# Performance work log

Hardware: AMD Instinct MI355X
Metric: run time of the kernel (lower is better)

Reference implementation:

```python
import jax, jax.numpy as jnp
import numpy as np

B, T, D, H = 32, 512, 1024, 1024


def setup_inputs() -> dict:
    key = jax.random.key(0)
    k1, k2, k3 = jax.random.split(key, 3)
    x = jax.random.normal(k1, (B, T, D), dtype=jnp.float32)
    c0 = jnp.zeros((B, H), dtype=jnp.float32)
    h0 = jnp.zeros((B, H), dtype=jnp.float32)
    # scale weights so gates do not saturate
    Wx = jax.random.normal(k2, (D, 4 * H), dtype=jnp.float32) * 0.05
    Wh = jax.random.normal(k3, (H, 4 * H), dtype=jnp.float32) * 0.05
    b = jnp.zeros((4 * H,), dtype=jnp.float32)
    return {"x": x, "c0": c0, "h0": h0, "Wx": Wx, "Wh": Wh, "b": b}


def reference(x, c0, h0, Wx, Wh, b):
    # Flax LSTMCell: gates = x @ Wx + h @ Wh + b, split into i,f,g,o.
    # Precompute the input projection for all timesteps (one big GEMM).
    xW = jnp.einsum('btd,dg->btg', x, Wx) + b  # [B,T,4H]

    def step(carry, xw_t):
        c, h = carry
        gates = xw_t + h @ Wh  # [B,4H]
        i, f, g, o = jnp.split(gates, 4, axis=-1)
        i = jax.nn.sigmoid(i)
        f = jax.nn.sigmoid(f)
        g = jnp.tanh(g)
        o = jax.nn.sigmoid(o)
        c_new = f * c + i * g
        h_new = o * jnp.tanh(c_new)
        return (c_new, h_new), h_new

    (cT, hT), ys = jax.lax.scan(step, (c0, h0), jnp.swapaxes(xW, 0, 1))
    outputs = jnp.swapaxes(ys, 0, 1)  # [B,T,H]
    return outputs, (cT, hT)
```

## Files before the change

kernel.cpp:

```cpp
#include <hip/hip_runtime.h>
#include <cstddef>

#define NB 32
#define NT 512
#define ND 1024
#define NH 1024
#define NG 4096
#define GRID 256

typedef unsigned short ushortT;
typedef unsigned long long u64;
typedef __attribute__((ext_vector_type(8))) short short8;
typedef __attribute__((ext_vector_type(4))) float f32x4;
typedef __attribute__((ext_vector_type(4))) unsigned uint4v;

#define GLL16(g, l) __builtin_amdgcn_global_load_lds(                      \
    (const __attribute__((address_space(1))) void*)(g),                    \
    (__attribute__((address_space(3))) void*)(l), 16, 0, 0)

__device__ __forceinline__ ushortT f2bf(float f) {
    union { float f; unsigned u; } v; v.f = f;
    unsigned r = v.u + 0x7FFFu + ((v.u >> 16) & 1u);
    return (ushortT)(r >> 16);
}
__device__ __forceinline__ float bf2f(ushortT u) {
    union { unsigned u; float f; } v; v.u = (unsigned)u << 16; return v.f;
}

__device__ __forceinline__ float pick4(float a0, float a1, float a2, float a3, int s) {
    float lo = (s & 1) ? a1 : a0;
    float hi = (s & 1) ? a3 : a2;
    return (s & 2) ? hi : lo;
}

__device__ __forceinline__ float fsigmoid(float x) {
    return __builtin_amdgcn_rcpf(1.f + __expf(-x));
}
__device__ __forceinline__ float ftanh(float x) {
    float xc = fminf(fmaxf(x, -15.f), 15.f);
    float e  = __expf(-2.f * xc);
    return (1.f - e) * __builtin_amdgcn_rcpf(1.f + e);
}

__global__ __launch_bounds__(256) void cast_bf16(const float* __restrict__ src,
                                                 ushortT* __restrict__ dst, int n4)
{
    int i = blockIdx.x * 256 + threadIdx.x;
    if (i < n4) {
        float4 v = ((const float4*)src)[i];
        ushort4 o;
        o.x = f2bf(v.x); o.y = f2bf(v.y); o.z = f2bf(v.z); o.w = f2bf(v.w);
        ((ushort4*)dst)[i] = o;
    }
}

__global__ __launch_bounds__(256) void transpose_cast(
    const float* __restrict__ src, ushortT* __restrict__ dst, int permute)
{
    __shared__ ushortT tile[64][66];
    const int c0 = blockIdx.x * 64, r0 = blockIdx.y * 64;
    const int cc = threadIdx.x & 63, rq = threadIdx.x >> 6;
    #pragma unroll
    for (int ps = 0; ps < 16; ++ps) {
        int r = ps * 4 + rq;
        tile[cc][r] = f2bf(src[(size_t)(r0 + r) * NG + c0 + cc]);
    }
    __syncthreads();
    #pragma unroll
    for (int ps = 0; ps < 16; ++ps) {
        int cl = ps * 4 + rq;
        int n  = c0 + cl;
        int drow = permute ? ((((n & 1023) >> 2) << 4) | ((n >> 10) << 2) | (n & 3))
                           : n;
        dst[(size_t)drow * 1024 + r0 + cc] = tile[cl][cc];
    }
}

__global__ __launch_bounds__(256) void gemm_xw_mfma(
    const ushortT* __restrict__ xb,
    const ushortT* __restrict__ wxT,
    const float* __restrict__ bias,
    ushortT* __restrict__ XWPb,
    int t0, int Tc, int tcsh)
{
    __shared__ ushortT As[128 * 32];
    __shared__ ushortT Bs[128 * 32];

    const int tid  = threadIdx.x;
    const int lane = tid & 63;
    const int wv   = tid >> 6;
    const int wr   = wv >> 1, wc = wv & 1;
    const int n0   = blockIdx.x * 128;
    const int m0   = blockIdx.y * 128;

    const int c1 = tid, c2 = tid + 256;
    const int rm1 = m0 + (c1 >> 2), rm2 = m0 + (c2 >> 2);
    const int xr1 = ((rm1 >> tcsh) * NT) + t0 + (rm1 & (Tc - 1));
    const int xr2 = ((rm2 >> tcsh) * NT) + t0 + (rm2 & (Tc - 1));
    const ushortT* ap1 = xb + (size_t)xr1 * ND + (c1 & 3) * 8;
    const ushortT* ap2 = xb + (size_t)xr2 * ND + (c2 & 3) * 8;
    const ushortT* bp1 = wxT + (size_t)(n0 + (c1 >> 2)) * ND + (c1 & 3) * 8;
    const ushortT* bp2 = wxT + (size_t)(n0 + (c2 >> 2)) * ND + (c2 & 3) * 8;

    f32x4 acc[4][4];
    #pragma unroll
    for (int m = 0; m < 4; ++m)
        #pragma unroll
        for (int n = 0; n < 4; ++n) acc[m][n] = (f32x4){0.f, 0.f, 0.f, 0.f};

    const int arow_base = (wr * 64 + (lane & 15)) * 32 + (lane >> 4) * 8;
    const int brow_base = (wc * 64 + (lane & 15)) * 32 + (lane >> 4) * 8;

    for (int k0 = 0; k0 < ND; k0 += 32) {
        __syncthreads();
        GLL16(ap1 + k0, &As[c1 * 8]);
        GLL16(ap2 + k0, &As[c2 * 8]);
        GLL16(bp1 + k0, &Bs[c1 * 8]);
        GLL16(bp2 + k0, &Bs[c2 * 8]);
        __syncthreads();
        short8 af[4], bf[4];
        #pragma unroll
        for (int m = 0; m < 4; ++m)
            af[m] = *(const short8*)&As[arow_base + m * 16 * 32];
        #pragma unroll
        for (int n = 0; n < 4; ++n)
            bf[n] = *(const short8*)&Bs[brow_base + n * 16 * 32];
        #pragma unroll
        for (int m = 0; m < 4; ++m)
            #pragma unroll
            for (int n = 0; n < 4; ++n)
                acc[m][n] = __builtin_amdgcn_mfma_f32_16x16x32_bf16(
                    af[m], bf[n], acc[m][n], 0, 0, 0);
    }

    #pragma unroll
    for (int n = 0; n < 4; ++n) {
        int col = n0 + wc * 64 + n * 16 + (lane & 15);
        int pc  = (((col & 1023) >> 2) << 4) | ((col >> 10) << 2) | (col & 3);
        float bs = bias[col];
        #pragma unroll
        for (int m = 0; m < 4; ++m) {
            #pragma unroll
            for (int r = 0; r < 4; ++r) {
                int rm = m0 + wr * 64 + m * 16 + (lane >> 4) * 4 + r;
                int b  = rm >> tcsh, tr = rm & (Tc - 1);
                XWPb[((size_t)tr * NB + b) * NG + pc] = f2bf(acc[m][n][r] + bs);
            }
        }
    }
}

__global__ __launch_bounds__(512) void lstm_persist(
    const ushortT* __restrict__ XWPb,
    const ushortT* __restrict__ whpT,
    unsigned* __restrict__ hb0,
    unsigned* __restrict__ hb1,
    const float* __restrict__ cinit,
    float* __restrict__ cT,
    float* __restrict__ out,
    float* __restrict__ hT,
    unsigned* __restrict__ flags,
    int t0, int Tc)
{
    __shared__ float red[2][16 * 272];

    const int tid  = threadIdx.x;
    const int lane = tid & 63;
    const int w    = tid >> 6;
    const int grp  = blockIdx.x & 1;
    const int s    = blockIdx.x >> 1;

    const int lo = lane & 15;
    const int hi = lane >> 4;

    const int rrow  = tid >> 5;
    const int col32 = tid & 31;
    const int rct   = col32 >> 4, rc16 = col32 & 15;
    const int gq    = (col32 >> 2) & 3;
    const int uu    = (col32 >> 4) * 4 + (col32 & 3);
    const int j     = s * 8 + uu;
    const int brow  = grp * 16 + rrow;

    short8 Bf[2][4];
    #pragma unroll
    for (int ct = 0; ct < 2; ++ct)
        #pragma unroll
        for (int ks = 0; ks < 4; ++ks)
            Bf[ct][ks] = *(const short8*)(whpT
                + (size_t)(s * 32 + ct * 16 + lo) * NH + w * 128 + ks * 32 + hi * 8);

    float creg = cinit[(size_t)brow * NH + j];

    const size_t abase64 = (size_t)lo * 256 + w * 32 + hi * 2;

    unsigned* const gf = flags + grp * 1024;
    const u64* fp = (const u64*)(gf + 128 * w + 2 * lane);
    unsigned* const fmine = gf + s * 8 + w;

    ushortT xvr = XWPb[(size_t)brow * NG + s * 32 + col32];

    const int tend = t0 + Tc;
    for (int t = t0; t < tend; ++t) {
        const int trel = t - t0;
        const int par  = t & 1;
        const unsigned* hR = ((t & 1) ? hb0 : hb1) + grp * 8192;
        unsigned*       hW = ((t & 1) ? hb1 : hb0) + grp * 8192;

        if (trel) {
            const unsigned tgt = (unsigned)trel;
            for (int it = 0; it < (1 << 17); ++it) {
                u64 v = __hip_atomic_load(fp, __ATOMIC_RELAXED,
                                          __HIP_MEMORY_SCOPE_AGENT);
                bool ok = ((unsigned)v >= tgt) && ((unsigned)(v >> 32) >= tgt);
                if (__all(ok)) break;
            }
        }

        const u64* ap = (const u64*)hR + abase64;
        u64 q0, q1;
        uint4v d0, d1, d2, d3;
        q0 = __hip_atomic_load(ap + 0,  __ATOMIC_RELAXED, __HIP_MEMORY_SCOPE_AGENT);
        q1 = __hip_atomic_load(ap + 1,  __ATOMIC_RELAXED, __HIP_MEMORY_SCOPE_AGENT);
        d0 = (uint4v){(unsigned)q0, (unsigned)(q0 >> 32), (unsigned)q1, (unsigned)(q1 >> 32)};
        q0 = __hip_atomic_load(ap + 8,  __ATOMIC_RELAXED, __HIP_MEMORY_SCOPE_AGENT);
        q1 = __hip_atomic_load(ap + 9,  __ATOMIC_RELAXED, __HIP_MEMORY_SCOPE_AGENT);
        d1 = (uint4v){(unsigned)q0, (unsigned)(q0 >> 32), (unsigned)q1, (unsigned)(q1 >> 32)};
        q0 = __hip_atomic_load(ap + 16, __ATOMIC_RELAXED, __HIP_MEMORY_SCOPE_AGENT);
        q1 = __hip_atomic_load(ap + 17, __ATOMIC_RELAXED, __HIP_MEMORY_SCOPE_AGENT);
        d2 = (uint4v){(unsigned)q0, (unsigned)(q0 >> 32), (unsigned)q1, (unsigned)(q1 >> 32)};
        q0 = __hip_atomic_load(ap + 24, __ATOMIC_RELAXED, __HIP_MEMORY_SCOPE_AGENT);
        q1 = __hip_atomic_load(ap + 25, __ATOMIC_RELAXED, __HIP_MEMORY_SCOPE_AGENT);
        d3 = (uint4v){(unsigned)q0, (unsigned)(q0 >> 32), (unsigned)q1, (unsigned)(q1 >> 32)};

        short8 A0 = *(short8*)&d0;
        short8 A1 = *(short8*)&d1;
        short8 A2 = *(short8*)&d2;
        short8 A3 = *(short8*)&d3;

        f32x4 acc0 = (f32x4){0.f, 0.f, 0.f, 0.f};
        f32x4 acc1 = (f32x4){0.f, 0.f, 0.f, 0.f};
        acc0 = __builtin_amdgcn_mfma_f32_16x16x32_bf16(A0, Bf[0][0], acc0, 0, 0, 0);
        acc1 = __builtin_amdgcn_mfma_f32_16x16x32_bf16(A0, Bf[1][0], acc1, 0, 0, 0);
        acc0 = __builtin_amdgcn_mfma_f32_16x16x32_bf16(A1, Bf[0][1], acc0, 0, 0, 0);
        acc1 = __builtin_amdgcn_mfma_f32_16x16x32_bf16(A1, Bf[1][1], acc1, 0, 0, 0);
        acc0 = __builtin_amdgcn_mfma_f32_16x16x32_bf16(A2, Bf[0][2], acc0, 0, 0, 0);
        acc1 = __builtin_amdgcn_mfma_f32_16x16x32_bf16(A2, Bf[1][2], acc1, 0, 0, 0);
        acc0 = __builtin_amdgcn_mfma_f32_16x16x32_bf16(A3, Bf[0][3], acc0, 0, 0, 0);
        acc1 = __builtin_amdgcn_mfma_f32_16x16x32_bf16(A3, Bf[1][3], acc1, 0, 0, 0);

        #pragma unroll
        for (int r = 0; r < 4; ++r) {
            red[par][(w * 2 + 0) * 272 + (hi * 4 + r) * 17 + lo] = acc0[r];
            red[par][(w * 2 + 1) * 272 + (hi * 4 + r) * 17 + lo] = acc1[r];
        }
        __syncthreads();

        float g = bf2f(xvr);
        #pragma unroll
        for (int wv = 0; wv < 8; ++wv)
            g += red[par][(wv * 2 + rct) * 272 + rrow * 17 + rc16];

        float g4  = __shfl_xor(g, 4);
        float g8  = __shfl_xor(g, 8);
        float g12 = __shfl_xor(g, 12);

        float gi = pick4(g, g4, g8, g12, gq);
        float gf = pick4(g, g4, g8, g12, gq ^ 1);
        float gg = pick4(g, g4, g8, g12, gq ^ 2);
        float go = pick4(g, g4, g8, g12, gq ^ 3);

        float iv = fsigmoid(gi);
        float fv = fsigmoid(gf);
        float gv = ftanh(gg);
        float ov = fsigmoid(go);
        float cn = fv * creg + iv * gv;
        float hn = ov * ftanh(cn);
        creg = cn;

        float ph = __shfl_xor(hn, 1);
        const bool wl = (gq == 0) && ((col32 & 1) == 0);
        if (wl) {
            unsigned pair = (unsigned)f2bf(hn) | ((unsigned)f2bf(ph) << 16);
            __hip_atomic_store(&hW[rrow * 512 + (j >> 1)], pair,
                               __ATOMIC_RELAXED, __HIP_MEMORY_SCOPE_AGENT);
        }

        if (t != tend - 1) {
            asm volatile("s_waitcnt vmcnt(0)" ::: "memory");
            if (lane == 0)
                __hip_atomic_store(fmine, (unsigned)(trel + 1),
                                   __ATOMIC_RELAXED, __HIP_MEMORY_SCOPE_AGENT);
            if (wl)
                *(float2*)&out[((size_t)brow * NT + t) * NH + j] = make_float2(hn, ph);
            xvr = XWPb[((size_t)(trel + 1) * NB + brow) * NG + s * 32 + col32];
        } else {
            if (wl)
                *(float2*)&out[((size_t)brow * NT + t) * NH + j] = make_float2(hn, ph);
            if (gq == 0) {
                if (t == NT - 1) hT[(size_t)brow * NH + j] = hn;
                cT[(size_t)brow * NH + j] = cn;
            }
        }
    }
}

extern "C" void kernel_launch(void* const* d_in, const int* in_sizes, int n_in,
                              void* d_out, int out_size, void* d_ws, size_t ws_size,
                              hipStream_t stream) {
    const float* x    = (const float*)d_in[0];
    const float* c0   = (const float*)d_in[1];
    const float* h0   = (const float*)d_in[2];
    const float* Wx   = (const float*)d_in[3];
    const float* Wh   = (const float*)d_in[4];
    const float* bias = (const float*)d_in[5];

    float* out = (float*)d_out;
    float* cT  = out + (size_t)NB * NT * NH;
    float* hT  = cT + (size_t)NB * NH;

    ushortT* xb   = (ushortT*)d_ws;
    ushortT* wxT  = xb  + (size_t)NB * NT * ND;
    ushortT* whpT = wxT + (size_t)NG * ND;
    unsigned* hb0 = (unsigned*)(whpT + (size_t)NG * NH);
    unsigned* hb1 = hb0 + NB * NH / 2;
    unsigned* flags = hb1 + NB * NH / 2;
    ushortT* xwpb = (ushortT*)(flags + 2 * 1024);

    const size_t fixed = ((size_t)NB * NT * ND + (size_t)NG * ND + (size_t)NG * NH
                          + 2 * NB * NH) * sizeof(ushortT) + 2 * 1024 * 4 + 256;
    int Tc = 512;
    while (Tc > 4 && fixed + (size_t)NB * Tc * NG * sizeof(ushortT) > ws_size)
        Tc >>= 1;
    int tcsh = 31 - __builtin_clz(Tc);

    cast_bf16<<<(NB * NT * ND / 4 + 255) / 256, 256, 0, stream>>>(x, xb, NB * NT * ND / 4);
    cast_bf16<<<(NB * NH / 4 + 255) / 256, 256, 0, stream>>>(h0, (ushortT*)hb1, NB * NH / 4);
    transpose_cast<<<dim3(64, 16), 256, 0, stream>>>(Wx, wxT, 0);
    transpose_cast<<<dim3(64, 16), 256, 0, stream>>>(Wh, whpT, 1);

    for (int t0 = 0; t0 < NT; t0 += Tc) {
        dim3 g(NG / 128, (NB * Tc) / 128);
        gemm_xw_mfma<<<g, 256, 0, stream>>>(xb, wxT, bias, xwpb, t0, Tc, tcsh);
        hipMemsetAsync(flags, 0, 2 * 1024 * sizeof(unsigned), stream);
        lstm_persist<<<GRID, 512, 0, stream>>>(
            xwpb, whpT, hb0, hb1,
            (t0 == 0) ? c0 : (const float*)cT,
            cT, out, hT, flags, t0, Tc);
    }
}
```

Baseline: 2.312 ms.

## Repartition persistent LSTM blocks to own gate columns across both batch halves

Each persistent block now owns 16 gate columns (4 hidden units) for all 32 batch rows, instead of 32 gate columns for one 16-row batch half. Each timestep runs as two phases, one per batch half, each with its own flag wait, h-buffer half and LDS reduction. This halves the per-block recurrent weight fragments and the MFMA work per phase. The aim is to interleave the two independent batch chains so one half's wait overlaps the other's compute. In exchange it adds a second barrier and flag poll per step, serializes both chains through every block, and leaves only half the threads active in the elementwise stage.

```diff
diff --git a/kernel.cpp b/kernel.cpp
--- a/kernel.cpp
+++ b/kernel.cpp
@@ -162,144 +162,153 @@
     unsigned* __restrict__ flags,
     int t0, int Tc)
 {
-    __shared__ float red[2][16 * 272];
+    __shared__ float red[2][8 * 16 * 17];
 
     const int tid  = threadIdx.x;
     const int lane = tid & 63;
     const int w    = tid >> 6;
-    const int grp  = blockIdx.x & 1;
-    const int s    = blockIdx.x >> 1;
+    const int blk  = blockIdx.x;
 
     const int lo = lane & 15;
     const int hi = lane >> 4;
 
-    const int rrow  = tid >> 5;
-    const int col32 = tid & 31;
-    const int rct   = col32 >> 4, rc16 = col32 & 15;
-    const int gq    = (col32 >> 2) & 3;
-    const int uu    = (col32 >> 4) * 4 + (col32 & 3);
-    const int j     = s * 8 + uu;
-    const int brow  = grp * 16 + rrow;
-
-    short8 Bf[2][4];
-    #pragma unroll
-    for (int ct = 0; ct < 2; ++ct)
-        #pragma unroll
-        for (int ks = 0; ks < 4; ++ks)
-            Bf[ct][ks] = *(const short8*)(whpT
-                + (size_t)(s * 32 + ct * 16 + lo) * NH + w * 128 + ks * 32 + hi * 8);
-
-    float creg = cinit[(size_t)brow * NH + j];
-
-    const size_t abase64 = (size_t)lo * 256 + w * 32 + hi * 2;
-
-    unsigned* const gf = flags + grp * 1024;
-    const u64* fp = (const u64*)(gf + 128 * w + 2 * lane);
-    unsigned* const fmine = gf + s * 8 + w;
-
-    ushortT xvr = XWPb[(size_t)brow * NG + s * 32 + col32];
+    short8 Bf[4];
+    #pragma unroll
+    for (int ks = 0; ks < 4; ++ks)
+        Bf[ks] = *(const short8*)(whpT
+            + (size_t)(blk * 16 + lo) * NH + w * 128 + ks * 32 + hi * 8);
+
+    const int rrow = (tid >> 4) & 15;
+    const int col  = tid & 15;
+    const int gq   = col >> 2;
+    const int jj   = col & 3;
+    const int j    = blk * 4 + jj;
+
+    float cregA = 0.f, cregB = 0.f;
+    if (tid < 256) {
+        cregA = cinit[(size_t)rrow * NH + j];
+        cregB = cinit[(size_t)(16 + rrow) * NH + j];
+    }
+
+    const size_t abase64 = (size_t)lo * 256 + 32 * w + 2 * hi;
+
+    const u64* fpollA = (const u64*)(flags + 0 * 1024 + 128 * w + 2 * lane);
+    const u64* fpollB = (const u64*)(flags + 1 * 1024 + 128 * w + 2 * lane);
+    unsigned* const fmineA = flags + 0 * 1024 + blk * 4 + w;
+    unsigned* const fmineB = flags + 1 * 1024 + blk * 4 + w;
+
+    ushortT xvrA = 0, xvrB = 0;
+    if (tid < 256) {
+        xvrA = XWPb[(size_t)rrow * NG + blk * 16 + col];
+        xvrB = XWPb[(size_t)(16 + rrow) * NG + blk * 16 + col];
+    }
 
     const int tend = t0 + Tc;
     for (int t = t0; t < tend; ++t) {
         const int trel = t - t0;
-        const int par  = t & 1;
-        const unsigned* hR = ((t & 1) ? hb0 : hb1) + grp * 8192;
-        unsigned*       hW = ((t & 1) ? hb1 : hb0) + grp * 8192;
-
-        if (trel) {
-            const unsigned tgt = (unsigned)trel;
-            for (int it = 0; it < (1 << 17); ++it) {
-                u64 v = __hip_atomic_load(fp, __ATOMIC_RELAXED,
-                                          __HIP_MEMORY_SCOPE_AGENT);
-                bool ok = ((unsigned)v >= tgt) && ((unsigned)(v >> 32) >= tgt);
-                if (__all(ok)) break;
+        const unsigned* hRg = (t & 1) ? hb0 : hb1;
+        unsigned*       hWg = (t & 1) ? hb1 : hb0;
+
+        #pragma unroll
+        for (int ph = 0; ph < 2; ++ph) {
+            const unsigned* hR = hRg + ph * 8192;
+            unsigned*       hW = hWg + ph * 8192;
+            const u64* fp = ph ? fpollB : fpollA;
+
+            if (trel) {
+                const unsigned tgt = (unsigned)trel;
+                for (int it = 0; it < (1 << 17); ++it) {
+                    u64 v = __hip_atomic_load(fp, __ATOMIC_RELAXED,
+                                              __HIP_MEMORY_SCOPE_AGENT);
+                    bool ok = ((unsigned)v >= tgt) && ((unsigned)(v >> 32) >= tgt);
+                    if (__all(ok)) break;
+                }
+            }
+
+            const u64* ap = (const u64*)hR + abase64;
+            u64 q0, q1;
+            uint4v d0, d1, d2, d3;
+            q0 = __hip_atomic_load(ap + 0,  __ATOMIC_RELAXED, __HIP_MEMORY_SCOPE_AGENT);
+            q1 = __hip_atomic_load(ap + 1,  __ATOMIC_RELAXED, __HIP_MEMORY_SCOPE_AGENT);
+            d0 = (uint4v){(unsigned)q0, (unsigned)(q0 >> 32), (unsigned)q1, (unsigned)(q1 >> 32)};
+            q0 = __hip_atomic_load(ap + 8,  __ATOMIC_RELAXED, __HIP_MEMORY_SCOPE_AGENT);
+            q1 = __hip_atomic_load(ap + 9,  __ATOMIC_RELAXED, __HIP_MEMORY_SCOPE_AGENT);
+            d1 = (uint4v){(unsigned)q0, (unsigned)(q0 >> 32), (unsigned)q1, (unsigned)(q1 >> 32)};
+            q0 = __hip_atomic_load(ap + 16, __ATOMIC_RELAXED, __HIP_MEMORY_SCOPE_AGENT);
+            q1 = __hip_atomic_load(ap + 17, __ATOMIC_RELAXED, __HIP_MEMORY_SCOPE_AGENT);
+            d2 = (uint4v){(unsigned)q0, (unsigned)(q0 >> 32), (unsigned)q1, (unsigned)(q1 >> 32)};
+            q0 = __hip_atomic_load(ap + 24, __ATOMIC_RELAXED, __HIP_MEMORY_SCOPE_AGENT);
+            q1 = __hip_atomic_load(ap + 25, __ATOMIC_RELAXED, __HIP_MEMORY_SCOPE_AGENT);
+            d3 = (uint4v){(unsigned)q0, (unsigned)(q0 >> 32), (unsigned)q1, (unsigned)(q1 >> 32)};
+
+            short8 A0 = *(short8*)&d0;
+            short8 A1 = *(short8*)&d1;
+            short8 A2 = *(short8*)&d2;
+            short8 A3 = *(short8*)&d3;
+
+            f32x4 acc0 = (f32x4){0.f, 0.f, 0.f, 0.f};
+            f32x4 acc1 = (f32x4){0.f, 0.f, 0.f, 0.f};
+            acc0 = __builtin_amdgcn_mfma_f32_16x16x32_bf16(A0, Bf[0], acc0, 0, 0, 0);
+            acc1 = __builtin_amdgcn_mfma_f32_16x16x32_bf16(A1, Bf[1], acc1, 0, 0, 0);
+            acc0 = __builtin_amdgcn_mfma_f32_16x16x32_bf16(A2, Bf[2], acc0, 0, 0, 0);
+            acc1 = __builtin_amdgcn_mfma_f32_16x16x32_bf16(A3, Bf[3], acc1, 0, 0, 0);
+
+            #pragma unroll
+            for (int r = 0; r < 4; ++r)
+                red[ph][(w * 16 + hi * 4 + r) * 17 + lo] = acc0[r] + acc1[r];
+            __syncthreads();
+
+            if (tid < 256) {
+                float xv = bf2f(ph ? xvrB : xvrA);
+                float g = xv;
+                #pragma unroll
+                for (int wv = 0; wv < 8; ++wv)
+                    g += red[ph][(wv * 16 + rrow) * 17 + col];
+
+                float g4  = __shfl_xor(g, 4);
+                float g8  = __shfl_xor(g, 8);
+                float g12 = __shfl_xor(g, 12);
+
+                float gi = pick4(g, g4, g8, g12, gq);
+                float gf = pick4(g, g4, g8, g12, gq ^ 1);
+                float gg = pick4(g, g4, g8, g12, gq ^ 2);
+                float go = pick4(g, g4, g8, g12, gq ^ 3);
+
+                float iv = fsigmoid(gi);
+                float fv = fsigmoid(gf);
+                float gv = ftanh(gg);
+                float ov = fsigmoid(go);
+                float creg = ph ? cregB : cregA;
+                float cn = fv * creg + iv * gv;
+                float hn = ov * ftanh(cn);
+                if (ph) cregB = cn; else cregA = cn;
+
+                float p2 = __shfl_xor(hn, 1);
+                const bool wl = (gq == 0) && ((col & 1) == 0);
+                const int brow = ph * 16 + rrow;
+                if (wl) {
+                    unsigned pair = (unsigned)f2bf(hn) | ((unsigned)f2bf(p2) << 16);
+                    __hip_atomic_store(&hW[rrow * 512 + 2 * blk + (col >> 1)], pair,
+                                       __ATOMIC_RELAXED, __HIP_MEMORY_SCOPE_AGENT);
+                    *(float2*)&out[((size_t)brow * NT + t) * NH + j] = make_float2(hn, p2);
+                }
+                if (t == tend - 1 && gq == 0) {
+                    if (t == NT - 1) hT[(size_t)brow * NH + j] = hn;
+                    cT[(size_t)brow * NH + j] = cn;
+                }
+                if (t != tend - 1) {
+                    asm volatile("s_waitcnt vmcnt(0)" ::: "memory");
+                    if (lane == 0)
+                        __hip_atomic_store(ph ? fmineB : fmineA,
+                                           (unsigned)(trel + 1),
+                                           __ATOMIC_RELAXED, __HIP_MEMORY_SCOPE_AGENT);
+                }
             }
         }
 
-        const u64* ap = (const u64*)hR + abase64;
-        u64 q0, q1;
-        uint4v d0, d1, d2, d3;
-        q0 = __hip_atomic_load(ap + 0,  __ATOMIC_RELAXED, __HIP_MEMORY_SCOPE_AGENT);
-        q1 = __hip_atomic_load(ap + 1,  __ATOMIC_RELAXED, __HIP_MEMORY_SCOPE_AGENT);
-        d0 = (uint4v){(unsigned)q0, (unsigned)(q0 >> 32), (unsigned)q1, (unsigned)(q1 >> 32)};
-        q0 = __hip_atomic_load(ap + 8,  __ATOMIC_RELAXED, __HIP_MEMORY_SCOPE_AGENT);
-        q1 = __hip_atomic_load(ap + 9,  __ATOMIC_RELAXED, __HIP_MEMORY_SCOPE_AGENT);
-        d1 = (uint4v){(unsigned)q0, (unsigned)(q0 >> 32), (unsigned)q1, (unsigned)(q1 >> 32)};
-        q0 = __hip_atomic_load(ap + 16, __ATOMIC_RELAXED, __HIP_MEMORY_SCOPE_AGENT);
-        q1 = __hip_atomic_load(ap + 17, __ATOMIC_RELAXED, __HIP_MEMORY_SCOPE_AGENT);
-        d2 = (uint4v){(unsigned)q0, (unsigned)(q0 >> 32), (unsigned)q1, (unsigned)(q1 >> 32)};
-        q0 = __hip_atomic_load(ap + 24, __ATOMIC_RELAXED, __HIP_MEMORY_SCOPE_AGENT);
-        q1 = __hip_atomic_load(ap + 25, __ATOMIC_RELAXED, __HIP_MEMORY_SCOPE_AGENT);
-        d3 = (uint4v){(unsigned)q0, (unsigned)(q0 >> 32), (unsigned)q1, (unsigned)(q1 >> 32)};
-
-        short8 A0 = *(short8*)&d0;
-        short8 A1 = *(short8*)&d1;
-        short8 A2 = *(short8*)&d2;
-        short8 A3 = *(short8*)&d3;
-
-        f32x4 acc0 = (f32x4){0.f, 0.f, 0.f, 0.f};
-        f32x4 acc1 = (f32x4){0.f, 0.f, 0.f, 0.f};
-        acc0 = __builtin_amdgcn_mfma_f32_16x16x32_bf16(A0, Bf[0][0], acc0, 0, 0, 0);
-        acc1 = __builtin_amdgcn_mfma_f32_16x16x32_bf16(A0, Bf[1][0], acc1, 0, 0, 0);
-        acc0 = __builtin_amdgcn_mfma_f32_16x16x32_bf16(A1, Bf[0][1], acc0, 0, 0, 0);
-        acc1 = __builtin_amdgcn_mfma_f32_16x16x32_bf16(A1, Bf[1][1], acc1, 0, 0, 0);
-        acc0 = __builtin_amdgcn_mfma_f32_16x16x32_bf16(A2, Bf[0][2], acc0, 0, 0, 0);
-        acc1 = __builtin_amdgcn_mfma_f32_16x16x32_bf16(A2, Bf[1][2], acc1, 0, 0, 0);
-        acc0 = __builtin_amdgcn_mfma_f32_16x16x32_bf16(A3, Bf[0][3], acc0, 0, 0, 0);
-        acc1 = __builtin_amdgcn_mfma_f32_16x16x32_bf16(A3, Bf[1][3], acc1, 0, 0, 0);
-
-        #pragma unroll
-        for (int r = 0; r < 4; ++r) {
-            red[par][(w * 2 + 0) * 272 + (hi * 4 + r) * 17 + lo] = acc0[r];
-            red[par][(w * 2 + 1) * 272 + (hi * 4 + r) * 17 + lo] = acc1[r];
-        }
-        __syncthreads();
-
-        float g = bf2f(xvr);
-        #pragma unroll
-        for (int wv = 0; wv < 8; ++wv)
-            g += red[par][(wv * 2 + rct) * 272 + rrow * 17 + rc16];
-
-        float g4  = __shfl_xor(g, 4);
-        float g8  = __shfl_xor(g, 8);
-        float g12 = __shfl_xor(g, 12);
-
-        float gi = pick4(g, g4, g8, g12, gq);
-        float gf = pick4(g, g4, g8, g12, gq ^ 1);
-        float gg = pick4(g, g4, g8, g12, gq ^ 2);
-        float go = pick4(g, g4, g8, g12, gq ^ 3);
-
-        float iv = fsigmoid(gi);
-        float fv = fsigmoid(gf);
-        float gv = ftanh(gg);
-        float ov = fsigmoid(go);
-        float cn = fv * creg + iv * gv;
-        float hn = ov * ftanh(cn);
-        creg = cn;
-
-        float ph = __shfl_xor(hn, 1);
-        const bool wl = (gq == 0) && ((col32 & 1) == 0);
-        if (wl) {
-            unsigned pair = (unsigned)f2bf(hn) | ((unsigned)f2bf(ph) << 16);
-            __hip_atomic_store(&hW[rrow * 512 + (j >> 1)], pair,
-                               __ATOMIC_RELAXED, __HIP_MEMORY_SCOPE_AGENT);
-        }
-
-        if (t != tend - 1) {
-            asm volatile("s_waitcnt vmcnt(0)" ::: "memory");
-            if (lane == 0)
-                __hip_atomic_store(fmine, (unsigned)(trel + 1),
-                                   __ATOMIC_RELAXED, __HIP_MEMORY_SCOPE_AGENT);
-            if (wl)
-                *(float2*)&out[((size_t)brow * NT + t) * NH + j] = make_float2(hn, ph);
-            xvr = XWPb[((size_t)(trel + 1) * NB + brow) * NG + s * 32 + col32];
-        } else {
-            if (wl)
-                *(float2*)&out[((size_t)brow * NT + t) * NH + j] = make_float2(hn, ph);
-            if (gq == 0) {
-                if (t == NT - 1) hT[(size_t)brow * NH + j] = hn;
-                cT[(size_t)brow * NH + j] = cn;
-            }
+        if (t != tend - 1 && tid < 256) {
+            xvrA = XWPb[((size_t)(trel + 1) * NB + rrow) * NG + blk * 16 + col];
+            xvrB = XWPb[((size_t)(trel + 1) * NB + 16 + rrow) * NG + blk * 16 + col];
         }
     }
 }
```

Result: slower. 2.952 ms (+27.6%).
